# Optimization experiments

Measured on AMD Instinct MI355X. Metric: run time of the kernel, lower is better.

The kernel has to match this reference:

```python
import jax, jax.numpy as jnp
import numpy as np

D = 32          # latent_dim
ALPHA = 3.0


def setup_inputs() -> dict:
    key = jax.random.key(0)
    ks = jax.random.split(key, 8)
    B, N, T = 4, 2048, 288
    spatial_nodes = jax.random.normal(ks[0], (B, N, D), dtype=jnp.float32)
    temporal_nodes = jax.random.normal(ks[1], (B, T, D), dtype=jnp.float32)
    # ss graph params: Linear(D, D, bias=False) x2
    W_ss1 = jax.random.normal(ks[2], (D, D), dtype=jnp.float32) / np.sqrt(D)
    W_ss2 = jax.random.normal(ks[3], (D, D), dtype=jnp.float32) / np.sqrt(D)
    # st / ts relation MLPs: Linear(2D, 1) -> weight vector (2D,) + scalar bias
    w_st = jax.random.normal(ks[4], (2 * D,), dtype=jnp.float32) / np.sqrt(2 * D)
    b_st = jnp.zeros((), dtype=jnp.float32)
    w_ts = jax.random.normal(ks[5], (2 * D,), dtype=jnp.float32) / np.sqrt(2 * D)
    b_ts = jnp.zeros((), dtype=jnp.float32)
    return {
        "spatial_nodes": spatial_nodes,
        "temporal_nodes": temporal_nodes,
        "W_ss1": W_ss1,
        "W_ss2": W_ss2,
        "w_st": w_st,
        "b_st": b_st,
        "w_ts": w_ts,
        "b_ts": b_ts,
    }


def _pair_linear(x1, x2, w, b):
    """Linear(2D->1) over the concat of every (x1[n], x2[m]) pair, without
    materializing the [B, N1, N2, 2D] tiled tensor: splits the weight into
    two matvecs and a broadcast add. Same math as the torch tile+concat+Linear."""
    d = x1.shape[-1]
    s1 = x1 @ w[:d]   # [B, N1]
    s2 = x2 @ w[d:]   # [B, N2]
    return s1[:, :, None] + s2[:, None, :] + b  # [B, N1, N2]


def reference(spatial_nodes, temporal_nodes, W_ss1, W_ss2, w_st, b_st, w_ts, b_ts):
    B, N, d = spatial_nodes.shape
    T = temporal_nodes.shape[1]

    # base graph: inner products of all node embeddings (only tt block survives)
    node_embs = jnp.concatenate([spatial_nodes, temporal_nodes], axis=1)  # [B, N+T, D]
    adj = jnp.einsum('bnf,bmf->bnm', node_embs, node_embs)               # [B, N+T, N+T]

    # ss block: antisymmetric tanh graph (nn.Linear applies x @ W.T)
    nv1 = jnp.tanh(ALPHA * (spatial_nodes @ W_ss1.T))
    nv2 = jnp.tanh(ALPHA * (spatial_nodes @ W_ss2.T))
    m = jnp.einsum('bnf,bmf->bnm', nv1, nv2)
    ss_adj = jnp.tanh(m - jnp.swapaxes(m, 1, 2))

    # st / ts blocks: pairwise concat + Linear(2D->1), fused
    st_adj = _pair_linear(spatial_nodes, temporal_nodes, w_st, b_st)  # [B, N, T]
    ts_adj = _pair_linear(temporal_nodes, spatial_nodes, w_ts, b_ts)  # [B, T, N]

    adj = adj.at[:, :N, N:].set(st_adj)
    adj = adj.at[:, N:, :N].set(ts_adj)
    adj = adj.at[:, :N, :N].set(ss_adj)

    # tt_mask=True: upper-triangular (incl. diagonal) on the temporal-temporal block
    adj = adj.at[:, N:, N:].set(jnp.triu(adj[:, N:, N:]))

    # forward: tanh(relu(adj)). The per-batch nonzero edge extraction in the
    # torch code is a dense->COO repack of exactly this tensor (indices where
    # adj != 0, values = adj at those indices); the dense adj is the canonical
    adj = jnp.tanh(jax.nn.relu(adj))
    return adj
```

## Files before the change

### kernel.cpp

```cpp
#include <hip/hip_runtime.h>

#define NTOT 2336
#define NS   2048
#define NT   288
#define DD   32
#define BATCH 4
#define S2   ((size_t)NTOT * NTOT)

#define WS_NV2   (BATCH * NS * DD)
#define WS_SST1  (2 * BATCH * NS * DD)
#define WS_SST2  (WS_SST1 + BATCH * NS)
#define WS_STS1  (WS_SST2 + BATCH * NT)
#define WS_STS2  (WS_STS1 + BATCH * NT)

#define TILE   128
#define NTILE  (NS / TILE)
#define NPAIR  (NTILE * (NTILE + 1) / 2)
#define SS_BLOCKS (NPAIR * BATCH)
#define ST_BLOCKS 2304
#define TS_BLOCKS 2304
#define TT_BLOCKS 1296
#define GRID_BLOCKS (SS_BLOCKS + ST_BLOCKS + TS_BLOCKS + TT_BLOCKS)
#define LDST 136

__device__ __forceinline__ float fast_tanh(float x) {
    float e = __expf(2.0f * x);
    return 1.0f - 2.0f * __builtin_amdgcn_rcpf(e + 1.0f);
}
__device__ __forceinline__ float f_out(float x) {
    return fast_tanh(fmaxf(x, 0.0f));
}

__global__ void precompute_kernel(const float* __restrict__ S,
                                  const float* __restrict__ T,
                                  const float* __restrict__ W1,
                                  const float* __restrict__ W2,
                                  const float* __restrict__ w_st,
                                  const float* __restrict__ b_st,
                                  const float* __restrict__ w_ts,
                                  const float* __restrict__ b_ts,
                                  float* __restrict__ ws) {
    __shared__ float sW1[DD * DD];
    __shared__ float sW2[DD * DD];
    __shared__ float swst[2 * DD];
    __shared__ float swts[2 * DD];
    int tid = threadIdx.x;
    for (int i = tid; i < DD * DD; i += 256) { sW1[i] = W1[i]; sW2[i] = W2[i]; }
    if (tid < 2 * DD) { swst[tid] = w_st[tid]; swts[tid] = w_ts[tid]; }
    __syncthreads();

    float* nv1T  = ws;
    float* nv2T  = ws + WS_NV2;
    float* s_st1 = ws + WS_SST1;
    float* s_st2 = ws + WS_SST2;
    float* s_ts1 = ws + WS_STS1;
    float* s_ts2 = ws + WS_STS2;

    int idx = blockIdx.x * 256 + tid;
    if (idx < BATCH * NS) {
        int b = idx >> 11, n = idx & (NS - 1);
        const float* row = S + idx * DD;
        float r[DD];
        #pragma unroll
        for (int q = 0; q < 8; q++) {
            float4 v = ((const float4*)row)[q];
            r[q * 4 + 0] = v.x; r[q * 4 + 1] = v.y;
            r[q * 4 + 2] = v.z; r[q * 4 + 3] = v.w;
        }
        size_t base = (size_t)b * DD * NS + n;
        #pragma unroll
        for (int d = 0; d < DD; d++) {
            float a1 = 0.f, a2 = 0.f;
            #pragma unroll
            for (int k = 0; k < DD; k++) {
                a1 = fmaf(r[k], sW1[d * DD + k], a1);
                a2 = fmaf(r[k], sW2[d * DD + k], a2);
            }
            nv1T[base + (size_t)d * NS] = fast_tanh(3.0f * a1);
            nv2T[base + (size_t)d * NS] = fast_tanh(3.0f * a2);
        }
        float d1 = 0.f, d2 = 0.f;
        #pragma unroll
        for (int k = 0; k < DD; k++) {
            d1 = fmaf(r[k], swst[k], d1);
            d2 = fmaf(r[k], swts[DD + k], d2);
        }
        s_st1[idx] = d1 + b_st[0];
        s_ts2[idx] = d2;
    } else if (idx < BATCH * NS + BATCH * NT) {
        int t = idx - BATCH * NS;
        const float* row = T + t * DD;
        float r[DD];
        #pragma unroll
        for (int q = 0; q < 8; q++) {
            float4 v = ((const float4*)row)[q];
            r[q * 4 + 0] = v.x; r[q * 4 + 1] = v.y;
            r[q * 4 + 2] = v.z; r[q * 4 + 3] = v.w;
        }
        float d1 = 0.f, d2 = 0.f;
        #pragma unroll
        for (int k = 0; k < DD; k++) {
            d1 = fmaf(r[k], swst[DD + k], d1);
            d2 = fmaf(r[k], swts[k], d2);
        }
        s_st2[t] = d1;
        s_ts1[t] = d2 + b_ts[0];
    }
}

__global__ __launch_bounds__(256) void mega_kernel(const float* __restrict__ ws,
                                                   const float* __restrict__ T,
                                                   float* __restrict__ out) {
    __shared__ __align__(16) float sA1[16][LDST];
    __shared__ __align__(16) float sA2[16][LDST];
    __shared__ __align__(16) float sB1[16][LDST];
    __shared__ __align__(16) float sB2[16][LDST];

    int blk = blockIdx.x;
    int tid = threadIdx.x;

    if (blk < SS_BLOCKS) {
        int b = blk & 3;
        int p = blk >> 2;
        int ti = 0;
        while (p >= NTILE - ti) { p -= NTILE - ti; ti++; }
        int tj = ti + p;

        const float* nv1T = ws + (size_t)b * DD * NS;
        const float* nv2T = ws + WS_NV2 + (size_t)b * DD * NS;

        int tx = tid & 15, ty = tid >> 4;
        float acc[8][8] = {};

        #pragma unroll
        for (int ph = 0; ph < 2; ph++) {
            if (ph) __syncthreads();
            #pragma unroll
            for (int it = 0; it < 2; it++) {
                int idx = it * 256 + tid;
                int k   = idx >> 5;
                int c4  = (idx & 31) * 4;
                const float* g = nv1T + (size_t)(ph * 16 + k) * NS;
                const float* h = nv2T + (size_t)(ph * 16 + k) * NS;
                *(float4*)&sA1[k][c4] = *(const float4*)(g + ti * TILE + c4);
                *(float4*)&sA2[k][c4] = *(const float4*)(h + ti * TILE + c4);
                *(float4*)&sB1[k][c4] = *(const float4*)(h + tj * TILE + c4);
                *(float4*)&sB2[k][c4] = *(const float4*)(g + tj * TILE + c4);
            }
            __syncthreads();
            #pragma unroll
            for (int k = 0; k < 16; k++) {
                float4 a1l = *(const float4*)&sA1[k][ty * 4];
                float4 a1h = *(const float4*)&sA1[k][64 + ty * 4];
                float4 a2l = *(const float4*)&sA2[k][ty * 4];
                float4 a2h = *(const float4*)&sA2[k][64 + ty * 4];
                float4 b1l = *(const float4*)&sB1[k][tx * 4];
                float4 b1h = *(const float4*)&sB1[k][64 + tx * 4];
                float4 b2l = *(const float4*)&sB2[k][tx * 4];
                float4 b2h = *(const float4*)&sB2[k][64 + tx * 4];
                float av1[8] = { a1l.x,a1l.y,a1l.z,a1l.w, a1h.x,a1h.y,a1h.z,a1h.w };
                float av2[8] = { a2l.x,a2l.y,a2l.z,a2l.w, a2h.x,a2h.y,a2h.z,a2h.w };
                float bv1[8] = { b1l.x,b1l.y,b1l.z,b1l.w, b1h.x,b1h.y,b1h.z,b1h.w };
                float bv2[8] = { b2l.x,b2l.y,b2l.z,b2l.w, b2h.x,b2h.y,b2h.z,b2h.w };
                #pragma unroll
                for (int i = 0; i < 8; i++)
                    #pragma unroll
                    for (int j = 0; j < 8; j++) {
                        acc[i][j] = fmaf(av1[i],  bv1[j], acc[i][j]);
                        acc[i][j] = fmaf(-av2[i], bv2[j], acc[i][j]);
                    }
            }
        }

        #pragma unroll
        for (int i = 0; i < 8; i++)
            #pragma unroll
            for (int j = 0; j < 8; j++)
                acc[i][j] = fast_tanh(acc[i][j]);

        float* obase = out + (size_t)b * S2;
        #pragma unroll
        for (int i = 0; i < 8; i++) {
            int r = ti * TILE + ((i < 4) ? (ty * 4 + i) : (60 + ty * 4 + i));
            float4 v0 = { f_out(acc[i][0]), f_out(acc[i][1]), f_out(acc[i][2]), f_out(acc[i][3]) };
            float4 v1 = { f_out(acc[i][4]), f_out(acc[i][5]), f_out(acc[i][6]), f_out(acc[i][7]) };
            *(float4*)(obase + (size_t)r * NTOT + tj * TILE + tx * 4)      = v0;
            *(float4*)(obase + (size_t)r * NTOT + tj * TILE + 64 + tx * 4) = v1;
        }
        if (ti != tj) {
            #pragma unroll
            for (int j = 0; j < 8; j++) {
                int r = tj * TILE + ((j < 4) ? (tx * 4 + j) : (60 + tx * 4 + j));
                float4 v0 = { f_out(-acc[0][j]), f_out(-acc[1][j]), f_out(-acc[2][j]), f_out(-acc[3][j]) };
                float4 v1 = { f_out(-acc[4][j]), f_out(-acc[5][j]), f_out(-acc[6][j]), f_out(-acc[7][j]) };
                *(float4*)(obase + (size_t)r * NTOT + ti * TILE + ty * 4)      = v0;
                *(float4*)(obase + (size_t)r * NTOT + ti * TILE + 64 + ty * 4) = v1;
            }
        }
    } else if (blk < SS_BLOCKS + ST_BLOCKS) {
        const float* s_st1 = ws + WS_SST1;
        const float* s_st2 = ws + WS_SST2;
        int idx = (blk - SS_BLOCKS) * 256 + tid;
        int t4  = idx % (NT / 4);
        int row = idx / (NT / 4);
        int b   = row >> 11;
        int n   = row & (NS - 1);
        float  s1 = s_st1[row];
        float4 s2 = *(const float4*)(s_st2 + b * NT + t4 * 4);
        float4 v  = { f_out(s1 + s2.x), f_out(s1 + s2.y), f_out(s1 + s2.z), f_out(s1 + s2.w) };
        *(float4*)(out + (size_t)b * S2 + (size_t)n * NTOT + NS + t4 * 4) = v;
    } else if (blk < SS_BLOCKS + ST_BLOCKS + TS_BLOCKS) {
        const float* s_ts1 = ws + WS_STS1;
        const float* s_ts2 = ws + WS_STS2;
        int idx = (blk - SS_BLOCKS - ST_BLOCKS) * 256 + tid;
        int n4  = idx & 511;
        int row = idx >> 9;
        int b   = row / NT;
        int t   = row - b * NT;
        float  s1 = s_ts1[row];
        float4 s2 = *(const float4*)(s_ts2 + b * NS + n4 * 4);
        float4 v  = { f_out(s1 + s2.x), f_out(s1 + s2.y), f_out(s1 + s2.z), f_out(s1 + s2.w) };
        *(float4*)(out + (size_t)b * S2 + (size_t)(NS + t) * NTOT + n4 * 4) = v;
    } else {
        int idx = (blk - SS_BLOCKS - ST_BLOCKS - TS_BLOCKS) * 256 + tid;
        int j   = idx % NT;
        int rem = idx / NT;
        int i   = rem % NT;
        int b   = rem / NT;
        float o = 0.f;
        if (j >= i) {
            const float4* ri = (const float4*)(T + (b * NT + i) * DD);
            const float4* rj = (const float4*)(T + (b * NT + j) * DD);
            float acc = 0.f;
            #pragma unroll
            for (int q = 0; q < 8; q++) {
                float4 a = ri[q], c = rj[q];
                acc = fmaf(a.x, c.x, acc); acc = fmaf(a.y, c.y, acc);
                acc = fmaf(a.z, c.z, acc); acc = fmaf(a.w, c.w, acc);
            }
            o = f_out(acc);
        }
        out[(size_t)b * S2 + (size_t)(NS + i) * NTOT + NS + j] = o;
    }
}

extern "C" void kernel_launch(void* const* d_in, const int* in_sizes, int n_in,
                              void* d_out, int out_size, void* d_ws, size_t ws_size,
                              hipStream_t stream) {
    const float* S    = (const float*)d_in[0];
    const float* T    = (const float*)d_in[1];
    const float* W1   = (const float*)d_in[2];
    const float* W2   = (const float*)d_in[3];
    const float* w_st = (const float*)d_in[4];
    const float* b_st = (const float*)d_in[5];
    const float* w_ts = (const float*)d_in[6];
    const float* b_ts = (const float*)d_in[7];
    float* out = (float*)d_out;
    float* ws  = (float*)d_ws;

    precompute_kernel<<<37, 256, 0, stream>>>(S, T, W1, W2, w_st, b_st, w_ts, b_ts, ws);
    mega_kernel<<<GRID_BLOCKS, 256, 0, stream>>>(ws, T, out);
}
```

Measured before the change: 138.7 us.

## Store tanh projections as packed fp16 and use dot2 in the ss block

The precompute kernel now packs the tanh-projected spatial features into half2 pairs, halving the workspace footprint. The ss tile loop loads all 16 packed k-steps in a single stage and accumulates with fdot2 instructions, with the subtraction folded in by sign-flipping the A2 tile. The outer tanh(relu(tanh)) is replaced by a polynomial on an odd function so relu applies after it. This cuts FMA count, shared/global traffic and transcendental work, at the cost of fp16 precision in the inner products and polynomial approximation error.

Result: faster. 132.5 us (-4.5%).

```diff
diff --git a/kernel.cpp b/kernel.cpp
--- a/kernel.cpp
+++ b/kernel.cpp
@@ -4,11 +4,14 @@
 #define NS   2048
 #define NT   288
 #define DD   32
+#define KK   16
 #define BATCH 4
 #define S2   ((size_t)NTOT * NTOT)
 
-#define WS_NV2   (BATCH * NS * DD)
-#define WS_SST1  (2 * BATCH * NS * DD)
+typedef _Float16 half2_t __attribute__((ext_vector_type(2)));
+
+#define WS_NV2H  (BATCH * KK * NS)
+#define WS_SST1  (2 * BATCH * KK * NS)
 #define WS_SST2  (WS_SST1 + BATCH * NS)
 #define WS_STS1  (WS_SST2 + BATCH * NT)
 #define WS_STS2  (WS_STS1 + BATCH * NT)
@@ -29,6 +32,20 @@
 }
 __device__ __forceinline__ float f_out(float x) {
     return fast_tanh(fmaxf(x, 0.0f));
+}
+__device__ __forceinline__ float poly_tanh01(float t) {
+    float t2 = t * t;
+    return t * fmaf(t2, fmaf(t2, 0.086330f, -0.324600f), 0.999905f);
+}
+__device__ __forceinline__ float fdot2(half2_t a, half2_t b, float c) {
+#if __has_builtin(__builtin_amdgcn_fdot2)
+    return __builtin_amdgcn_fdot2(a, b, c, false);
+#else
+    return c + (float)a.x * (float)b.x + (float)a.y * (float)b.y;
+#endif
+}
+__device__ __forceinline__ half2_t bc_h2(float f) {
+    return __builtin_bit_cast(half2_t, f);
 }
 
 __global__ void precompute_kernel(const float* __restrict__ S,
@@ -49,8 +66,8 @@
     if (tid < 2 * DD) { swst[tid] = w_st[tid]; swts[tid] = w_ts[tid]; }
     __syncthreads();
 
-    float* nv1T  = ws;
-    float* nv2T  = ws + WS_NV2;
+    float* nv1h  = ws;
+    float* nv2h  = ws + WS_NV2H;
     float* s_st1 = ws + WS_SST1;
     float* s_st2 = ws + WS_SST2;
     float* s_ts1 = ws + WS_STS1;
@@ -67,7 +84,7 @@
             r[q * 4 + 0] = v.x; r[q * 4 + 1] = v.y;
             r[q * 4 + 2] = v.z; r[q * 4 + 3] = v.w;
         }
-        size_t base = (size_t)b * DD * NS + n;
+        float o1[DD], o2[DD];
         #pragma unroll
         for (int d = 0; d < DD; d++) {
             float a1 = 0.f, a2 = 0.f;
@@ -76,8 +93,16 @@
                 a1 = fmaf(r[k], sW1[d * DD + k], a1);
                 a2 = fmaf(r[k], sW2[d * DD + k], a2);
             }
-            nv1T[base + (size_t)d * NS] = fast_tanh(3.0f * a1);
-            nv2T[base + (size_t)d * NS] = fast_tanh(3.0f * a2);
+            o1[d] = fast_tanh(3.0f * a1);
+            o2[d] = fast_tanh(3.0f * a2);
+        }
+        size_t base = (size_t)b * KK * NS + n;
+        #pragma unroll
+        for (int kk = 0; kk < KK; kk++) {
+            half2_t h1 = { (_Float16)o1[2 * kk], (_Float16)o1[2 * kk + 1] };
+            half2_t h2 = { (_Float16)o2[2 * kk], (_Float16)o2[2 * kk + 1] };
+            nv1h[base + (size_t)kk * NS] = __builtin_bit_cast(float, h1);
+            nv2h[base + (size_t)kk * NS] = __builtin_bit_cast(float, h2);
         }
         float d1 = 0.f, d2 = 0.f;
         #pragma unroll
@@ -111,10 +136,10 @@
 __global__ __launch_bounds__(256) void mega_kernel(const float* __restrict__ ws,
                                                    const float* __restrict__ T,
                                                    float* __restrict__ out) {
-    __shared__ __align__(16) float sA1[16][LDST];
-    __shared__ __align__(16) float sA2[16][LDST];
-    __shared__ __align__(16) float sB1[16][LDST];
-    __shared__ __align__(16) float sB2[16][LDST];
+    __shared__ __align__(16) float sA1[KK][LDST];
+    __shared__ __align__(16) float sA2[KK][LDST];
+    __shared__ __align__(16) float sB1[KK][LDST];
+    __shared__ __align__(16) float sB2[KK][LDST];
 
     int blk = blockIdx.x;
     int tid = threadIdx.x;
@@ -126,64 +151,71 @@
         while (p >= NTILE - ti) { p -= NTILE - ti; ti++; }
         int tj = ti + p;
 
-        const float* nv1T = ws + (size_t)b * DD * NS;
-        const float* nv2T = ws + WS_NV2 + (size_t)b * DD * NS;
+        const float* nv1h = ws + (size_t)b * KK * NS;
+        const float* nv2h = ws + WS_NV2H + (size_t)b * KK * NS;
+
+        #pragma unroll
+        for (int it = 0; it < 2; it++) {
+            int idx = it * 256 + tid;
+            int kk  = idx >> 5;
+            int c4  = (idx & 31) * 4;
+            const float* g1 = nv1h + (size_t)kk * NS;
+            const float* g2 = nv2h + (size_t)kk * NS;
+            *(float4*)&sA1[kk][c4] = *(const float4*)(g1 + ti * TILE + c4);
+            float4 v = *(const float4*)(g2 + ti * TILE + c4);
+            uint4 uv = *(uint4*)&v;
+            uv.x ^= 0x80008000u; uv.y ^= 0x80008000u;
+            uv.z ^= 0x80008000u; uv.w ^= 0x80008000u;
+            *(uint4*)&sA2[kk][c4] = uv;
+            *(float4*)&sB1[kk][c4] = *(const float4*)(g2 + tj * TILE + c4);
+            *(float4*)&sB2[kk][c4] = *(const float4*)(g1 + tj * TILE + c4);
+        }
+        __syncthreads();
 
         int tx = tid & 15, ty = tid >> 4;
         float acc[8][8] = {};
 
-        #pragma unroll
-        for (int ph = 0; ph < 2; ph++) {
-            if (ph) __syncthreads();
-            #pragma unroll
-            for (int it = 0; it < 2; it++) {
-                int idx = it * 256 + tid;
-                int k   = idx >> 5;
-                int c4  = (idx & 31) * 4;
-                const float* g = nv1T + (size_t)(ph * 16 + k) * NS;
-                const float* h = nv2T + (size_t)(ph * 16 + k) * NS;
-                *(float4*)&sA1[k][c4] = *(const float4*)(g + ti * TILE + c4);
-                *(float4*)&sA2[k][c4] = *(const float4*)(h + ti * TILE + c4);
-                *(float4*)&sB1[k][c4] = *(const float4*)(h + tj * TILE + c4);
-                *(float4*)&sB2[k][c4] = *(const float4*)(g + tj * TILE + c4);
-            }
-            __syncthreads();
-            #pragma unroll
-            for (int k = 0; k < 16; k++) {
-                float4 a1l = *(const float4*)&sA1[k][ty * 4];
-                float4 a1h = *(const float4*)&sA1[k][64 + ty * 4];
-                float4 a2l = *(const float4*)&sA2[k][ty * 4];
-                float4 a2h = *(const float4*)&sA2[k][64 + ty * 4];
-                float4 b1l = *(const float4*)&sB1[k][tx * 4];
-                float4 b1h = *(const float4*)&sB1[k][64 + tx * 4];
-                float4 b2l = *(const float4*)&sB2[k][tx * 4];
-                float4 b2h = *(const float4*)&sB2[k][64 + tx * 4];
-                float av1[8] = { a1l.x,a1l.y,a1l.z,a1l.w, a1h.x,a1h.y,a1h.z,a1h.w };
-                float av2[8] = { a2l.x,a2l.y,a2l.z,a2l.w, a2h.x,a2h.y,a2h.z,a2h.w };
-                float bv1[8] = { b1l.x,b1l.y,b1l.z,b1l.w, b1h.x,b1h.y,b1h.z,b1h.w };
-                float bv2[8] = { b2l.x,b2l.y,b2l.z,b2l.w, b2h.x,b2h.y,b2h.z,b2h.w };
+        #pragma unroll 4
+        for (int kk = 0; kk < KK; kk++) {
+            float4 a1l = *(const float4*)&sA1[kk][ty * 4];
+            float4 a1h = *(const float4*)&sA1[kk][64 + ty * 4];
+            float4 a2l = *(const float4*)&sA2[kk][ty * 4];
+            float4 a2h = *(const float4*)&sA2[kk][64 + ty * 4];
+            float4 b1l = *(const float4*)&sB1[kk][tx * 4];
+            float4 b1h = *(const float4*)&sB1[kk][64 + tx * 4];
+            float4 b2l = *(const float4*)&sB2[kk][tx * 4];
+            float4 b2h = *(const float4*)&sB2[kk][64 + tx * 4];
+            half2_t av1[8] = { bc_h2(a1l.x), bc_h2(a1l.y), bc_h2(a1l.z), bc_h2(a1l.w),
+                               bc_h2(a1h.x), bc_h2(a1h.y), bc_h2(a1h.z), bc_h2(a1h.w) };
+            half2_t av2[8] = { bc_h2(a2l.x), bc_h2(a2l.y), bc_h2(a2l.z), bc_h2(a2l.w),
+                               bc_h2(a2h.x), bc_h2(a2h.y), bc_h2(a2h.z), bc_h2(a2h.w) };
+            half2_t bv1[8] = { bc_h2(b1l.x), bc_h2(b1l.y), bc_h2(b1l.z), bc_h2(b1l.w),
+                               bc_h2(b1h.x), bc_h2(b1h.y), bc_h2(b1h.z), bc_h2(b1h.w) };
+            half2_t bv2[8] = { bc_h2(b2l.x), bc_h2(b2l.y), bc_h2(b2l.z), bc_h2(b2l.w),
+                               bc_h2(b2h.x), bc_h2(b2h.y), bc_h2(b2h.z), bc_h2(b2h.w) };
+            #pragma unroll
+            for (int i = 0; i < 8; i++)
                 #pragma unroll
-                for (int i = 0; i < 8; i++)
-                    #pragma unroll
-                    for (int j = 0; j < 8; j++) {
-                        acc[i][j] = fmaf(av1[i],  bv1[j], acc[i][j]);
-                        acc[i][j] = fmaf(-av2[i], bv2[j], acc[i][j]);
-                    }
-            }
+                for (int j = 0; j < 8; j++) {
+                    acc[i][j] = fdot2(av1[i], bv1[j], acc[i][j]);
+                    acc[i][j] = fdot2(av2[i], bv2[j], acc[i][j]);
+                }
         }
 
         #pragma unroll
         for (int i = 0; i < 8; i++)
             #pragma unroll
             for (int j = 0; j < 8; j++)
-                acc[i][j] = fast_tanh(acc[i][j]);
+                acc[i][j] = poly_tanh01(fast_tanh(acc[i][j]));
 
         float* obase = out + (size_t)b * S2;
         #pragma unroll
         for (int i = 0; i < 8; i++) {
             int r = ti * TILE + ((i < 4) ? (ty * 4 + i) : (60 + ty * 4 + i));
-            float4 v0 = { f_out(acc[i][0]), f_out(acc[i][1]), f_out(acc[i][2]), f_out(acc[i][3]) };
-            float4 v1 = { f_out(acc[i][4]), f_out(acc[i][5]), f_out(acc[i][6]), f_out(acc[i][7]) };
+            float4 v0 = { fmaxf(acc[i][0], 0.f), fmaxf(acc[i][1], 0.f),
+                          fmaxf(acc[i][2], 0.f), fmaxf(acc[i][3], 0.f) };
+            float4 v1 = { fmaxf(acc[i][4], 0.f), fmaxf(acc[i][5], 0.f),
+                          fmaxf(acc[i][6], 0.f), fmaxf(acc[i][7], 0.f) };
             *(float4*)(obase + (size_t)r * NTOT + tj * TILE + tx * 4)      = v0;
             *(float4*)(obase + (size_t)r * NTOT + tj * TILE + 64 + tx * 4) = v1;
         }
@@ -191,8 +223,10 @@
             #pragma unroll
             for (int j = 0; j < 8; j++) {
                 int r = tj * TILE + ((j < 4) ? (tx * 4 + j) : (60 + tx * 4 + j));
-                float4 v0 = { f_out(-acc[0][j]), f_out(-acc[1][j]), f_out(-acc[2][j]), f_out(-acc[3][j]) };
-                float4 v1 = { f_out(-acc[4][j]), f_out(-acc[5][j]), f_out(-acc[6][j]), f_out(-acc[7][j]) };
+                float4 v0 = { fmaxf(-acc[0][j], 0.f), fmaxf(-acc[1][j], 0.f),
+                              fmaxf(-acc[2][j], 0.f), fmaxf(-acc[3][j], 0.f) };
+                float4 v1 = { fmaxf(-acc[4][j], 0.f), fmaxf(-acc[5][j], 0.f),
+                              fmaxf(-acc[6][j], 0.f), fmaxf(-acc[7][j], 0.f) };
                 *(float4*)(obase + (size_t)r * NTOT + ti * TILE + ty * 4)      = v0;
                 *(float4*)(obase + (size_t)r * NTOT + ti * TILE + 64 + ty * 4) = v1;
             }
```
